# Performance work log

Hardware: AMD Instinct MI355X
Metric: run time of the kernel (lower is better)

The kernel has to match this reference:

```python
import jax, jax.numpy as jnp
import numpy as np

NEG_SLOPE = 0.01  # torch nn.LeakyReLU default

B, N, IN_F, OUT_F, HEADS = 4, 2048, 512, 512, 8
D = OUT_F // HEADS  # 64


def setup_inputs() -> dict:
    key = jax.random.key(0)
    ks = jax.random.split(key, 4)
    X = jax.random.normal(ks[0], (B, N, IN_F), dtype=jnp.float32)
    W_v = jax.random.normal(ks[1], (IN_F, D), dtype=jnp.float32) * (IN_F ** -0.5)
    b_v = jnp.zeros((D,), dtype=jnp.float32)
    W_q = jax.random.normal(ks[2], (D, HEADS), dtype=jnp.float32) * (D ** -0.5)
    b_q = jnp.zeros((HEADS,), dtype=jnp.float32)
    W_k = jax.random.normal(ks[3], (D, HEADS), dtype=jnp.float32) * (D ** -0.5)
    b_k = jnp.zeros((HEADS,), dtype=jnp.float32)
    return {"X": X, "W_v": W_v, "b_v": b_v, "W_q": W_q, "b_q": b_q, "W_k": W_k, "b_k": b_k}


def reference(X, W_v, b_v, W_q, b_q, W_k, b_k):
    # V: (B, N, D)
    V = X @ W_v + b_v
    # per-node, per-head scalar scores: (B, N, H) -> (B, H, N)
    Q = jnp.swapaxes(V @ W_q + b_q, 1, 2)
    K = jnp.swapaxes(V @ W_k + b_k, 1, 2)
    # A[b,h,i,j] = leaky_relu(Q[b,h,j] + K[b,h,i])  (broadcast outer-sum)
    A = jax.nn.leaky_relu(Q[:, :, None, :] + K[:, :, :, None], negative_slope=NEG_SLOPE)
    A = jax.nn.softmax(A, axis=-1)  # dropout = identity in eval mode
    # H[b,i,h,f] = sum_j A[b,h,i,j] V[b,j,f]
    H = jnp.einsum('bhij,bjf->bihf', A, V)
    return H.reshape(H.shape[0], H.shape[1], -1)  # (B, N, H*D)
```

## Files before the change

### kernel.cpp

```cpp
#include <hip/hip_runtime.h>

#define BB   4
#define NN   2048
#define INF  512
#define HH   8
#define DD   64
#define BH   (BB*HH)
#define NCK  16
#define CKS  128


__global__ __launch_bounds__(256) void k_vq(
    const float* __restrict__ X, const float* __restrict__ Wv,
    const float* __restrict__ bv,
    const float* __restrict__ Wq, const float* __restrict__ bq,
    const float* __restrict__ Wk, const float* __restrict__ bk,
    float* __restrict__ V, float* __restrict__ qsg, float* __restrict__ ksg,
    unsigned long long* __restrict__ qk64)
{
  __shared__ float Ws[2][64][68];
  __shared__ float red[128][16];
  __shared__ float Vs[32][65];
  const int t  = threadIdx.x;
  const int kh = t >> 7;
  const int u  = t & 127;
  const int tc = u & 15;
  const int rg = u >> 4;
  const int r0 = blockIdx.x * 32;
  const int k0 = kh * 256;
  float acc[4][4];
  #pragma unroll
  for (int r = 0; r < 4; r++)
    #pragma unroll
    for (int c = 0; c < 4; c++) acc[r][c] = 0.f;

  for (int kc = 0; kc < 256; kc += 64) {
    __syncthreads();
    #pragma unroll
    for (int i = 0; i < 8; i++) {
      const int e4 = u + i * 128;
      const int k  = e4 >> 4;
      const int n4 = (e4 & 15) * 4;
      *(float4*)(&Ws[kh][k][n4]) =
          *(const float4*)(Wv + (size_t)(k0 + kc + k) * DD + n4);
    }
    __syncthreads();
    const float* xp = X + (size_t)(r0 + rg * 4) * INF + k0 + kc;
    #pragma unroll 4
    for (int kk = 0; kk < 64; kk += 4) {
      float4 xr[4];
      #pragma unroll
      for (int r = 0; r < 4; r++)
        xr[r] = *(const float4*)(xp + (size_t)r * INF + kk);
      #pragma unroll
      for (int j = 0; j < 4; j++) {
        const float4 w4 = *(const float4*)(&Ws[kh][kk + j][tc * 4]);
        #pragma unroll
        for (int r = 0; r < 4; r++) {
          const float x = (j == 0) ? xr[r].x : (j == 1) ? xr[r].y
                        : (j == 2) ? xr[r].z : xr[r].w;
          acc[r][0] += x * w4.x;  acc[r][1] += x * w4.y;
          acc[r][2] += x * w4.z;  acc[r][3] += x * w4.w;
        }
      }
    }
  }

  __syncthreads();
  if (kh == 1) {
    #pragma unroll
    for (int r = 0; r < 4; r++)
      *(float4*)(&red[u][r * 4]) = *(const float4*)(&acc[r][0]);
  }
  __syncthreads();
  if (kh == 0) {
    const float4 bb = *(const float4*)(bv + tc * 4);
    #pragma unroll
    for (int r = 0; r < 4; r++) {
      const float4 p = *(const float4*)(&red[u][r * 4]);
      float4 o;
      o.x = acc[r][0] + p.x + bb.x;  o.y = acc[r][1] + p.y + bb.y;
      o.z = acc[r][2] + p.z + bb.z;  o.w = acc[r][3] + p.w + bb.w;
      *(float4*)(V + (size_t)(r0 + rg * 4 + r) * DD + tc * 4) = o;
      Vs[rg * 4 + r][tc * 4]     = o.x;  Vs[rg * 4 + r][tc * 4 + 1] = o.y;
      Vs[rg * 4 + r][tc * 4 + 2] = o.z;  Vs[rg * 4 + r][tc * 4 + 3] = o.w;
    }
  }
  __syncthreads();

  const int row = t >> 3;
  const int h   = t & 7;
  float sq = bq[h], sk = bk[h];
  #pragma unroll 8
  for (int dd = 0; dd < DD; dd++) {
    const float v = Vs[row][dd];
    sq += v * Wq[dd * HH + h];
    sk += v * Wk[dd * HH + h];
  }
  const int grow = r0 + row;
  const int b = grow >> 11, n = grow & (NN - 1);
  const int bh = b * HH + h;
  qsg[bh * NN + n] = sq;
  ksg[bh * NN + n] = sk;
  unsigned uo = __float_as_uint(sq);
  uo = (uo & 0x80000000u) ? ~uo : (uo | 0x80000000u);
  qk64[(size_t)bh * NN + n] = ((unsigned long long)uo << 32) | (unsigned)n;
}

__global__ __launch_bounds__(256) void k_rank(
    const unsigned long long* __restrict__ qk64,
    float* __restrict__ sqs, unsigned short* __restrict__ idxg)
{
  __shared__ __align__(16) unsigned long long keys[NN];
  __shared__ int cnt[4][256];
  const int t  = threadIdx.x;
  const int bh = blockIdx.x >> 3;
  const int jq = t & 63;
  const int kq = t >> 6;
  const unsigned long long* __restrict__ kb = qk64 + (size_t)bh * NN;

  {
    const ulonglong2* __restrict__ g2 = (const ulonglong2*)kb;
    ulonglong2* s2 = (ulonglong2*)keys;
    #pragma unroll
    for (int x = 0; x < 4; x++) s2[t + 256 * x] = g2[t + 256 * x];
  }
  __syncthreads();

  const int jg = ((blockIdx.x & 7) << 8) | (jq << 2);
  const unsigned long long kj0 = keys[jg];
  const unsigned long long kj1 = keys[jg + 1];
  const unsigned long long kj2 = keys[jg + 2];
  const unsigned long long kj3 = keys[jg + 3];

  const ulonglong2* __restrict__ k2 = (const ulonglong2*)(keys + kq * 512);
  int c0 = 0, c1 = 0, c2 = 0, c3 = 0;
  #pragma unroll 8
  for (int l = 0; l < 256; l++) {
    const ulonglong2 kk = k2[l];
    c0 += (kk.x < kj0) + (kk.y < kj0);
    c1 += (kk.x < kj1) + (kk.y < kj1);
    c2 += (kk.x < kj2) + (kk.y < kj2);
    c3 += (kk.x < kj3) + (kk.y < kj3);
  }
  cnt[kq][0 * 64 + jq] = c0;
  cnt[kq][1 * 64 + jq] = c1;
  cnt[kq][2 * 64 + jq] = c2;
  cnt[kq][3 * 64 + jq] = c3;
  __syncthreads();

  if (kq == 0) {
    #pragma unroll
    for (int u = 0; u < 4; u++) {
      const int rank = cnt[0][u * 64 + jq] + cnt[1][u * 64 + jq]
                     + cnt[2][u * 64 + jq] + cnt[3][u * 64 + jq];
      const unsigned long long kj = keys[jg + u];
      const unsigned uo = (unsigned)(kj >> 32);
      const unsigned ur = (uo & 0x80000000u) ? (uo & 0x7fffffffu) : ~uo;
      sqs [bh * NN + rank] = __uint_as_float(ur);
      idxg[bh * NN + rank] = (unsigned short)(jg + u);
    }
  }
}

__global__ __launch_bounds__(256) void k_scan(
    const float* __restrict__ sq, const unsigned short* __restrict__ idxg,
    const float* __restrict__ V,
    float* __restrict__ P1, float* __restrict__ P2,
    float* __restrict__ l1, float* __restrict__ l2,
    float* __restrict__ S1g, float* __restrict__ S2g,
    float* __restrict__ SL1, float* __restrict__ SL2)
{
  __shared__ float vstash[4][32][DD];
  __shared__ float ss1[4][64], ss2[4][64], sl1[4], sl2[4];
  const int t  = threadIdx.x;
  const int bh = blockIdx.x >> 4;
  const int ck = blockIdx.x & 15;
  const int d  = t & 63, g = t >> 6;
  const int r0 = ck*CKS + g*32;
  const float* Vb  = V + (size_t)(bh >> 3) * NN * DD;
  const float* sqb = sq + bh*NN;
  const unsigned short* ib = idxg + bh*NN;
  float a1 = 0.f, a2 = 0.f, s1 = 0.f, s2 = 0.f;
  #pragma unroll 8
  for (int rr = 0; rr < 32; rr++) {
    const int r = r0 + rr;
    const float qv = sqb[r];
    const float e1 = __expf(qv), e2 = __expf(0.01f*qv);
    const float v  = Vb[(size_t)ib[r]*DD + d];
    vstash[g][rr][d] = v;
    a1 += e1*v;  a2 += e2*v;  s1 += e1;  s2 += e2;
  }
  ss1[g][d] = a1;  ss2[g][d] = a2;
  if (d == 0) { sl1[g] = s1;  sl2[g] = s2; }
  __syncthreads();
  float o1 = 0.f, o2 = 0.f, lo1 = 0.f, lo2 = 0.f;
  for (int gg = 0; gg < g; gg++) { o1 += ss1[gg][d]; o2 += ss2[gg][d]; lo1 += sl1[gg]; lo2 += sl2[gg]; }
  if (g == 0) {
    S1g[(bh*NCK + ck)*64 + d] = ss1[0][d]+ss1[1][d]+ss1[2][d]+ss1[3][d];
    S2g[(bh*NCK + ck)*64 + d] = ss2[0][d]+ss2[1][d]+ss2[2][d]+ss2[3][d];
    if (d == 0) {
      SL1[bh*NCK + ck] = sl1[0]+sl1[1]+sl1[2]+sl1[3];
      SL2[bh*NCK + ck] = sl2[0]+sl2[1]+sl2[2]+sl2[3];
    }
  }
  a1 = o1; a2 = o2; s1 = lo1; s2 = lo2;
  float* P1b = P1 + (size_t)bh*NN*DD;
  float* P2b = P2 + (size_t)bh*NN*DD;
  #pragma unroll 8
  for (int rr = 0; rr < 32; rr++) {
    const int r = r0 + rr;
    const float qv = sqb[r];
    const float e1 = __expf(qv), e2 = __expf(0.01f*qv);
    const float v  = vstash[g][rr][d];
    P1b[(size_t)r*DD + d] = a1;
    P2b[(size_t)r*DD + d] = a2;
    if (d == 0) { l1[bh*NN + r] = s1;  l2[bh*NN + r] = s2; }
    a1 += e1*v;  a2 += e2*v;  s1 += e1;  s2 += e2;
  }
}

__global__ __launch_bounds__(256) void k_out(
    const float* __restrict__ sq, const float* __restrict__ ksg,
    const float* __restrict__ P1, const float* __restrict__ P2,
    const float* __restrict__ S1g, const float* __restrict__ S2g,
    const float* __restrict__ SL1, const float* __restrict__ SL2,
    const float* __restrict__ l1, const float* __restrict__ l2,
    float* __restrict__ out)
{
  __shared__ float Of1[NCK + 1][64], Of2[NCK + 1][64];
  __shared__ float Lo1[NCK + 1], Lo2[NCK + 1];
  const int t   = threadIdx.x;
  const int bh  = blockIdx.x >> 7;
  const int loc = blockIdx.x & 127;
  const int w   = t >> 6;
  const int d   = t & 63;
  const int i0  = loc*16 + w*4;
  const int b   = bh >> 3, h = bh & 7;

  if (t < 64) {
    float a = 0.f;
    for (int ck = 0; ck < NCK; ck++) {
      Of1[ck][t] = a;  a += S1g[(bh*NCK + ck)*64 + t];
    }
    Of1[NCK][t] = a;
  } else if (t < 128) {
    const int dd = t - 64;
    float a = 0.f;
    for (int ck = 0; ck < NCK; ck++) {
      Of2[ck][dd] = a;  a += S2g[(bh*NCK + ck)*64 + dd];
    }
    Of2[NCK][dd] = a;
  } else if (t == 128) {
    float a = 0.f;
    for (int ck = 0; ck < NCK; ck++) { Lo1[ck] = a;  a += SL1[bh*NCK + ck]; }
    Lo1[NCK] = a;
  } else if (t == 129) {
    float a = 0.f;
    for (int ck = 0; ck < NCK; ck++) { Lo2[ck] = a;  a += SL2[bh*NCK + ck]; }
    Lo2[NCK] = a;
  }
  __syncthreads();

  const float* s = sq + bh*NN;
  const float probe = s[d*32 + 31];
  const float T1  = Of1[NCK][d];
  const float Lt1 = Lo1[NCK];
  const size_t base = (size_t)bh * NN * DD;

  float kv[4], tt[4];
  int pos[4];
  #pragma unroll
  for (int u = 0; u < 4; u++) { kv[u] = ksg[bh*NN + i0 + u];  tt[u] = -kv[u]; }
  #pragma unroll
  for (int u = 0; u < 4; u++) {
    const unsigned long long m1 = __ballot(probe <= tt[u]);
    const int c1 = __popcll(m1);
    if (c1 == 64) pos[u] = NN;
    else {
      const unsigned long long m2 = __ballot(s[c1*32 + (d & 31)] <= tt[u]);
      pos[u] = c1*32 + (__popcll(m2) >> 1);
    }
  }
  #pragma unroll
  for (int u = 0; u < 4; u++) {
    const float ek  = __expf(kv[u]);
    const float ek2 = __expf(0.01f * kv[u]);
    float p1v, p2v, q1v, q2v;
    if (pos[u] < NN) {
      const int ch = pos[u] >> 7;
      p1v = P1[base + (size_t)pos[u]*DD + d] + Of1[ch][d];
      p2v = P2[base + (size_t)pos[u]*DD + d] + Of2[ch][d];
      q1v = l1[bh*NN + pos[u]] + Lo1[ch];
      q2v = l2[bh*NN + pos[u]] + Lo2[ch];
    } else {
      p1v = T1;   p2v = Of2[NCK][d];
      q1v = Lt1;  q2v = Lo2[NCK];
    }
    const float num = ek * (T1 - p1v)  + ek2 * p2v;
    const float den = ek * (Lt1 - q1v) + ek2 * q2v;
    out[((size_t)(b*NN + i0 + u)) * (HH*DD) + h*DD + d] = num / den;
  }
}

extern "C" void kernel_launch(void* const* d_in, const int* in_sizes, int n_in,
                              void* d_out, int out_size, void* d_ws, size_t ws_size,
                              hipStream_t stream)
{
  (void)in_sizes; (void)n_in; (void)out_size; (void)ws_size;
  const float* X  = (const float*)d_in[0];
  const float* Wv = (const float*)d_in[1];
  const float* bv = (const float*)d_in[2];
  const float* Wq = (const float*)d_in[3];
  const float* bq = (const float*)d_in[4];
  const float* Wk = (const float*)d_in[5];
  const float* bk = (const float*)d_in[6];
  float* out = (float*)d_out;

  float* w = (float*)d_ws;
  float* V     = w;  w += (size_t)BB*NN*DD;
  float* qsg   = w;  w += BH*NN;
  float* ksg   = w;  w += BH*NN;
  float* l1    = w;  w += BH*NN;
  float* l2    = w;  w += BH*NN;
  unsigned short* idxg = (unsigned short*)w;  w += BH*NN/2;
  float* S1g   = w;  w += (size_t)BH*NCK*DD;
  float* S2g   = w;  w += (size_t)BH*NCK*DD;
  float* SL1   = w;  w += BH*NCK;
  float* SL2   = w;  w += BH*NCK;
  float* sqs   = w;  w += BH*NN;
  unsigned long long* qk64 = (unsigned long long*)w;  w += BH*NN*2;
  float* P1    = w;  w += (size_t)BH*NN*DD;
  float* P2    = w;  w += (size_t)BH*NN*DD;

  k_vq   <<<256, 256, 0, stream>>>(X, Wv, bv, Wq, bq, Wk, bk, V, qsg, ksg, qk64);
  k_rank <<<BH*8, 256, 0, stream>>>(qk64, sqs, idxg);
  k_scan <<<BH*NCK, 256, 0, stream>>>(sqs, idxg, V, P1, P2, l1, l2, S1g, S2g, SL1, SL2);
  k_out  <<<BH*128, 256, 0, stream>>>(sqs, ksg, P1, P2, S1g, S2g, SL1, SL2, l1, l2, out);
}
```

Measured before the change: 133.7 us.

## Fuse scan and output into cooperative kernel with LDS-resident prefix sums

```diff
diff --git a/kernel.cpp b/kernel.cpp
--- a/kernel.cpp
+++ b/kernel.cpp
@@ -1,4 +1,6 @@
 #include <hip/hip_runtime.h>
+#include <hip/hip_cooperative_groups.h>
+namespace cg = cooperative_groups;
 
 #define BB   4
 #define NN   2048
@@ -15,7 +17,7 @@
     const float* __restrict__ bv,
     const float* __restrict__ Wq, const float* __restrict__ bq,
     const float* __restrict__ Wk, const float* __restrict__ bk,
-    float* __restrict__ V, float* __restrict__ qsg, float* __restrict__ ksg,
+    float* __restrict__ V, float* __restrict__ ksg,
     unsigned long long* __restrict__ qk64)
 {
   __shared__ float Ws[2][64][68];
@@ -100,7 +102,6 @@
   const int grow = r0 + row;
   const int b = grow >> 11, n = grow & (NN - 1);
   const int bh = b * HH + h;
-  qsg[bh * NN + n] = sq;
   ksg[bh * NN + n] = sk;
   unsigned uo = __float_as_uint(sq);
   uo = (uo & 0x80000000u) ? ~uo : (uo | 0x80000000u);
@@ -163,33 +164,49 @@
   }
 }
 
-__global__ __launch_bounds__(256) void k_scan(
-    const float* __restrict__ sq, const unsigned short* __restrict__ idxg,
-    const float* __restrict__ V,
-    float* __restrict__ P1, float* __restrict__ P2,
-    float* __restrict__ l1, float* __restrict__ l2,
+__global__ __launch_bounds__(256, 2) void k_so(
+    const float* __restrict__ sqs, const unsigned short* __restrict__ idxg,
+    const float* __restrict__ V, const float* __restrict__ ksg,
     float* __restrict__ S1g, float* __restrict__ S2g,
-    float* __restrict__ SL1, float* __restrict__ SL2)
+    float* __restrict__ SL1, float* __restrict__ SL2,
+    float* __restrict__ out)
 {
-  __shared__ float vstash[4][32][DD];
-  __shared__ float ss1[4][64], ss2[4][64], sl1[4], sl2[4];
+  __shared__ float P1l[CKS + 1][64];
+  __shared__ float P2l[CKS + 1][64];
+  __shared__ float sqc[CKS];
+  __shared__ float Ll1[CKS + 1], Ll2[CKS + 1];
+  __shared__ __align__(16) unsigned char scr[12304];
+  __shared__ int nwl;
+
+  float (*ss1)[64] = (float(*)[64])scr;
+  float (*ss2)[64] = (float(*)[64])(scr + 1024);
+  float* sl1 = (float*)(scr + 2048);
+  float* sl2 = (float*)(scr + 2064);
+  unsigned short* wl = (unsigned short*)scr;
+  float* kwl = (float*)(scr + 4096);
+
   const int t  = threadIdx.x;
   const int bh = blockIdx.x >> 4;
   const int ck = blockIdx.x & 15;
   const int d  = t & 63, g = t >> 6;
-  const int r0 = ck*CKS + g*32;
-  const float* Vb  = V + (size_t)(bh >> 3) * NN * DD;
-  const float* sqb = sq + bh*NN;
-  const unsigned short* ib = idxg + bh*NN;
+  const int r0 = ck * CKS + g * 32;
+  const int b  = bh >> 3, h = bh & 7;
+  const float* Vb  = V + (size_t)b * NN * DD;
+  const float* sqb = sqs + bh * NN;
+  const unsigned short* ib = idxg + bh * NN;
+
+  if (t < CKS) sqc[t] = sqb[ck * CKS + t];
+  if (t == 0) nwl = 0;
+
   float a1 = 0.f, a2 = 0.f, s1 = 0.f, s2 = 0.f;
   #pragma unroll 8
   for (int rr = 0; rr < 32; rr++) {
     const int r = r0 + rr;
     const float qv = sqb[r];
-    const float e1 = __expf(qv), e2 = __expf(0.01f*qv);
-    const float v  = Vb[(size_t)ib[r]*DD + d];
-    vstash[g][rr][d] = v;
-    a1 += e1*v;  a2 += e2*v;  s1 += e1;  s2 += e2;
+    const float e1 = __expf(qv), e2 = __expf(0.01f * qv);
+    const float v  = Vb[(size_t)ib[r] * DD + d];
+    P1l[g * 32 + rr][d] = v;
+    a1 += e1 * v;  a2 += e2 * v;  s1 += e1;  s2 += e2;
   }
   ss1[g][d] = a1;  ss2[g][d] = a2;
   if (d == 0) { sl1[g] = s1;  sl2[g] = s2; }
@@ -204,102 +221,70 @@
       SL2[bh*NCK + ck] = sl2[0]+sl2[1]+sl2[2]+sl2[3];
     }
   }
-  a1 = o1; a2 = o2; s1 = lo1; s2 = lo2;
-  float* P1b = P1 + (size_t)bh*NN*DD;
-  float* P2b = P2 + (size_t)bh*NN*DD;
+  a1 = o1;  a2 = o2;  s1 = lo1;  s2 = lo2;
   #pragma unroll 8
   for (int rr = 0; rr < 32; rr++) {
-    const int r = r0 + rr;
-    const float qv = sqb[r];
-    const float e1 = __expf(qv), e2 = __expf(0.01f*qv);
-    const float v  = vstash[g][rr][d];
-    P1b[(size_t)r*DD + d] = a1;
-    P2b[(size_t)r*DD + d] = a2;
-    if (d == 0) { l1[bh*NN + r] = s1;  l2[bh*NN + r] = s2; }
-    a1 += e1*v;  a2 += e2*v;  s1 += e1;  s2 += e2;
-  }
-}
-
-__global__ __launch_bounds__(256) void k_out(
-    const float* __restrict__ sq, const float* __restrict__ ksg,
-    const float* __restrict__ P1, const float* __restrict__ P2,
-    const float* __restrict__ S1g, const float* __restrict__ S2g,
-    const float* __restrict__ SL1, const float* __restrict__ SL2,
-    const float* __restrict__ l1, const float* __restrict__ l2,
-    float* __restrict__ out)
-{
-  __shared__ float Of1[NCK + 1][64], Of2[NCK + 1][64];
-  __shared__ float Lo1[NCK + 1], Lo2[NCK + 1];
-  const int t   = threadIdx.x;
-  const int bh  = blockIdx.x >> 7;
-  const int loc = blockIdx.x & 127;
-  const int w   = t >> 6;
-  const int d   = t & 63;
-  const int i0  = loc*16 + w*4;
-  const int b   = bh >> 3, h = bh & 7;
-
-  if (t < 64) {
-    float a = 0.f;
-    for (int ck = 0; ck < NCK; ck++) {
-      Of1[ck][t] = a;  a += S1g[(bh*NCK + ck)*64 + t];
-    }
-    Of1[NCK][t] = a;
-  } else if (t < 128) {
-    const int dd = t - 64;
-    float a = 0.f;
-    for (int ck = 0; ck < NCK; ck++) {
-      Of2[ck][dd] = a;  a += S2g[(bh*NCK + ck)*64 + dd];
-    }
-    Of2[NCK][dd] = a;
-  } else if (t == 128) {
-    float a = 0.f;
-    for (int ck = 0; ck < NCK; ck++) { Lo1[ck] = a;  a += SL1[bh*NCK + ck]; }
-    Lo1[NCK] = a;
-  } else if (t == 129) {
-    float a = 0.f;
-    for (int ck = 0; ck < NCK; ck++) { Lo2[ck] = a;  a += SL2[bh*NCK + ck]; }
-    Lo2[NCK] = a;
-  }
-  __syncthreads();
-
-  const float* s = sq + bh*NN;
-  const float probe = s[d*32 + 31];
-  const float T1  = Of1[NCK][d];
-  const float Lt1 = Lo1[NCK];
-  const size_t base = (size_t)bh * NN * DD;
-
-  float kv[4], tt[4];
-  int pos[4];
+    const int row = g * 32 + rr;
+    const float qv = sqb[r0 + rr];
+    const float e1 = __expf(qv), e2 = __expf(0.01f * qv);
+    const float v  = P1l[row][d];
+    P1l[row][d] = a1;
+    P2l[row][d] = a2;
+    if (d == 0) { Ll1[row] = s1;  Ll2[row] = s2; }
+    a1 += e1 * v;  a2 += e2 * v;  s1 += e1;  s2 += e2;
+  }
+  if (g == 3) {
+    P1l[CKS][d] = a1;  P2l[CKS][d] = a2;
+    if (d == 0) { Ll1[CKS] = s1;  Ll2[CKS] = s2; }
+  }
+  __threadfence();
+  cg::this_grid().sync();
+
+  float of1 = 0.f, of2 = 0.f, t1 = 0.f, t2 = 0.f;
+  float so1 = 0.f, so2 = 0.f, lt1 = 0.f, lt2 = 0.f;
   #pragma unroll
-  for (int u = 0; u < 4; u++) { kv[u] = ksg[bh*NN + i0 + u];  tt[u] = -kv[u]; }
+  for (int c2 = 0; c2 < NCK; c2++) {
+    const float v1 = S1g[(bh*NCK + c2)*64 + d];
+    const float v2 = S2g[(bh*NCK + c2)*64 + d];
+    const float w1 = SL1[bh*NCK + c2];
+    const float w2 = SL2[bh*NCK + c2];
+    t1 += v1;  t2 += v2;  lt1 += w1;  lt2 += w2;
+    if (c2 < ck) { of1 += v1; of2 += v2; so1 += w1; so2 += w2; }
+  }
+  const float qlo = ck ? sqb[ck * CKS - 1] : -__builtin_inff();
+  const float qhi = (ck < NCK - 1) ? sqc[CKS - 1] : __builtin_inff();
+
+  const float* kb = ksg + bh * NN;
   #pragma unroll
-  for (int u = 0; u < 4; u++) {
-    const unsigned long long m1 = __ballot(probe <= tt[u]);
-    const int c1 = __popcll(m1);
-    if (c1 == 64) pos[u] = NN;
-    else {
-      const unsigned long long m2 = __ballot(s[c1*32 + (d & 31)] <= tt[u]);
-      pos[u] = c1*32 + (__popcll(m2) >> 1);
-    }
-  }
-  #pragma unroll
-  for (int u = 0; u < 4; u++) {
-    const float ek  = __expf(kv[u]);
-    const float ek2 = __expf(0.01f * kv[u]);
-    float p1v, p2v, q1v, q2v;
-    if (pos[u] < NN) {
-      const int ch = pos[u] >> 7;
-      p1v = P1[base + (size_t)pos[u]*DD + d] + Of1[ch][d];
-      p2v = P2[base + (size_t)pos[u]*DD + d] + Of2[ch][d];
-      q1v = l1[bh*NN + pos[u]] + Lo1[ch];
-      q2v = l2[bh*NN + pos[u]] + Lo2[ch];
-    } else {
-      p1v = T1;   p2v = Of2[NCK][d];
-      q1v = Lt1;  q2v = Lo2[NCK];
-    }
-    const float num = ek * (T1 - p1v)  + ek2 * p2v;
-    const float den = ek * (Lt1 - q1v) + ek2 * q2v;
-    out[((size_t)(b*NN + i0 + u)) * (HH*DD) + h*DD + d] = num / den;
+  for (int s = 0; s < 8; s++) {
+    const int i = t + 256 * s;
+    const float kv = kb[i];
+    const float tt = -kv;
+    if (qlo <= tt && tt < qhi) {
+      const int slot = atomicAdd(&nwl, 1);
+      wl[slot]  = (unsigned short)i;
+      kwl[slot] = kv;
+    }
+  }
+  __syncthreads();
+
+  const int n = nwl;
+  for (int e = g; e < n; e += 4) {
+    const int i = wl[e];
+    const float kv = kwl[e];
+    const float tt = -kv;
+    const unsigned long long b0 = __ballot(sqc[d] <= tt);
+    const unsigned long long b1 = __ballot(sqc[64 + d] <= tt);
+    const int loc = __popcll(b0) + __popcll(b1);
+    const float p1v = of1 + P1l[loc][d];
+    const float p2v = of2 + P2l[loc][d];
+    const float q1v = so1 + Ll1[loc];
+    const float q2v = so2 + Ll2[loc];
+    const float ek  = __expf(kv);
+    const float ek2 = __expf(0.01f * kv);
+    const float num = ek * (t1  - p1v) + ek2 * p2v;
+    const float den = ek * (lt1 - q1v) + ek2 * q2v;
+    out[((size_t)(b * NN + i)) * (HH * DD) + h * DD + d] = num / den;
   }
 }
 
@@ -319,10 +304,7 @@
 
   float* w = (float*)d_ws;
   float* V     = w;  w += (size_t)BB*NN*DD;
-  float* qsg   = w;  w += BH*NN;
   float* ksg   = w;  w += BH*NN;
-  float* l1    = w;  w += BH*NN;
-  float* l2    = w;  w += BH*NN;
   unsigned short* idxg = (unsigned short*)w;  w += BH*NN/2;
   float* S1g   = w;  w += (size_t)BH*NCK*DD;
   float* S2g   = w;  w += (size_t)BH*NCK*DD;
@@ -330,11 +312,13 @@
   float* SL2   = w;  w += BH*NCK;
   float* sqs   = w;  w += BH*NN;
   unsigned long long* qk64 = (unsigned long long*)w;  w += BH*NN*2;
-  float* P1    = w;  w += (size_t)BH*NN*DD;
-  float* P2    = w;  w += (size_t)BH*NN*DD;
-
-  k_vq   <<<256, 256, 0, stream>>>(X, Wv, bv, Wq, bq, Wk, bk, V, qsg, ksg, qk64);
+
+  k_vq   <<<256, 256, 0, stream>>>(X, Wv, bv, Wq, bq, Wk, bk, V, ksg, qk64);
   k_rank <<<BH*8, 256, 0, stream>>>(qk64, sqs, idxg);
-  k_scan <<<BH*NCK, 256, 0, stream>>>(sqs, idxg, V, P1, P2, l1, l2, S1g, S2g, SL1, SL2);
-  k_out  <<<BH*128, 256, 0, stream>>>(sqs, ksg, P1, P2, S1g, S2g, SL1, SL2, l1, l2, out);
+
+  void* args[] = { (void*)&sqs, (void*)&idxg, (void*)&V, (void*)&ksg,
+                   (void*)&S1g, (void*)&S2g, (void*)&SL1, (void*)&SL2,
+                   (void*)&out };
+  hipLaunchCooperativeKernel((const void*)k_so, dim3(BH*NCK), dim3(256),
+                             args, 0, stream);
 }
```

After: 215.1 us. 60.9% more time.
